# Optimization experiments

Hardware: AMD Instinct MI355X
Metric: run time of the kernel (lower is better)

The kernel has to match this reference:

```python
import jax, jax.numpy as jnp
import numpy as np

N_NODE = 50000
N_EDGE = 800000
D_FEAT = 64
DEPTH = 3
STEP = 0.5
AB_TUPLES = [(0.0, float(b)) for b in np.arange(0, 3, STEP)] + [(float(a), 0.0) for a in np.arange(STEP, 3, STEP)]
M = len(AB_TUPLES)  # 11 bases
L_INT, R_INT = -1.0, 1.0  # Jacobi spectral interval [l, r]


def setup_inputs() -> dict:
    key = jax.random.key(0)
    k1, k2, k3 = jax.random.split(key, 3)
    x = jax.random.normal(k1, (N_NODE, D_FEAT), dtype=jnp.float32)
    edge_index = jax.random.randint(k2, (2, N_EDGE), 0, N_NODE, dtype=jnp.int32)
    edge_attr = jax.random.uniform(k3, (N_EDGE,), dtype=jnp.float32)
    alphas = jnp.ones((DEPTH, M), dtype=jnp.float32)  # base_alpha = min(1/alpha, 1) = 1.0
    w = jnp.ones((1, M, 1, 1), dtype=jnp.float32)
    a_arr = jnp.array([t[0] for t in AB_TUPLES], dtype=jnp.float32)
    b_arr = jnp.array([t[1] for t in AB_TUPLES], dtype=jnp.float32)
    return {"x": x, "edge_index": edge_index, "edge_attr": edge_attr,
            "alphas": alphas, "w": w, "a_arr": a_arr, "b_arr": b_arr}


def _forward(x, edge_index, edge_attr, alphas, w, a_arr, b_arr):
    row, col = edge_index[0], edge_index[1]
    # gcn normalization: out-degree of row index, isolated nodes bumped to 1
    deg = jax.ops.segment_sum(jnp.ones_like(edge_attr), row, num_segments=N_NODE)
    deg = jnp.where(deg < 0.5, deg + 1.0, deg)
    dinv = deg ** -0.5
    val = dinv[row] * edge_attr * dinv[col]

    def spmm_all(xs):  # xs: [M, N, D] -> adj @ xs[m] for each basis (sequential map bounds memory)
        return jax.lax.map(
            lambda xm: jax.ops.segment_sum(val[:, None] * xm[col], row, num_segments=N_NODE), xs)

    a = a_arr[:, None, None]  # [M,1,1]
    b = b_arr[:, None, None]
    l, r = L_INT, R_INT
    xs0 = jnp.broadcast_to(x, (M,) + x.shape)  # order-0 term, shared across bases
    xs_hist = [xs0]
    # L = 1 Jacobi term
    coef1 = (a - b) / 2 - (a + b + 2) / 2 * (l + r) / (r - l)
    coef2 = (a + b + 2) / (r - l)
    al0 = alphas[0][:, None, None]
    xs_hist.append(al0 * (coef1 * xs0 + coef2 * spmm_all(xs0)))
    # L >= 2 three-term Jacobi recurrence
    for Lk in range(2, DEPTH + 1):
        Lf = float(Lk)
        coef_l = 2 * Lf * (Lf + a + b) * (2 * Lf - 2 + a + b)
        coef_lm1_1 = (2 * Lf + a + b - 1) * (2 * Lf + a + b) * (2 * Lf + a + b - 2)
        coef_lm1_2 = (2 * Lf + a + b - 1) * (a * a - b * b)
        coef_lm2 = 2 * (Lf - 1 + a) * (Lf - 1 + b) * (2 * Lf + a + b)
        alL = alphas[Lk - 1][:, None, None]
        alLm1 = alphas[Lk - 2][:, None, None]
        tmp1 = alL * (coef_lm1_1 / coef_l)
        tmp2 = alL * (coef_lm1_2 / coef_l)
        tmp3 = alL * alLm1 * (coef_lm2 / coef_l)
        tmp1_2 = tmp1 * (2 / (r - l))
        tmp2_2 = tmp1 * ((r + l) / (r - l)) + tmp2
        nx = tmp1_2 * spmm_all(xs_hist[-1]) - tmp2_2 * xs_hist[-1] - tmp3 * xs_hist[-2]
        xs_hist.append(nx)
    h = jnp.stack(xs_hist, axis=0)       # [K, M, N, D]
    h = jnp.transpose(h, (2, 1, 0, 3))   # [N, M, K, D], matches torch stack(dim=1) then stack(dim=2)
    return (w * h).sum(axis=1)           # [N, K, D]


def reference(x, edge_index, edge_attr, alphas, w, a_arr, b_arr):
    return _forward(x, edge_index, edge_attr, alphas, w, a_arr, b_arr)
```

## Files before the change

kernel.cpp:

```cpp
#include <hip/hip_runtime.h>
#include <hip/hip_fp16.h>

#define NN 50000
#define NE 800000
#define DF 64
#define MM 11
#define OUT_K 4
#define PAD 16
#define SLAB_CAP (NE + (PAD - 1) * NN + 64)

__device__ __forceinline__ float bf2f(unsigned short u) {
    union { unsigned int i; float f; } v; v.i = ((unsigned int)u) << 16; return v.f;
}
__device__ __forceinline__ unsigned short f2bf(float f) {
    union { float f; unsigned int i; } v; v.f = f;
    unsigned int u = v.i + 0x7FFFu + ((v.i >> 16) & 1u);
    return (unsigned short)(u >> 16);
}


__global__ void k_deg(const int* __restrict__ row, int* __restrict__ deg) {
    int e = blockIdx.x * blockDim.x + threadIdx.x;
    if (e < NE) atomicAdd(&deg[row[e]], 1);
}

__global__ void k_alloc(const int* __restrict__ deg, int* __restrict__ counter,
                        int* __restrict__ rowstart, float* __restrict__ dinv,
                        const float* __restrict__ alphas, const float* __restrict__ w,
                        const float* __restrict__ a_arr, const float* __restrict__ b_arr,
                        float* __restrict__ gamma) {
    int i = blockIdx.x * blockDim.x + threadIdx.x;
    int lane = threadIdx.x & 63;
    int d = (i < NN) ? deg[i] : 0;
    int dp = (d + PAD - 1) & ~(PAD - 1);
    int v = dp;
    #pragma unroll
    for (int off = 1; off < 64; off <<= 1) {
        int t = __shfl_up(v, off, 64);
        if (lane >= off) v += t;
    }
    int total = __shfl(v, 63, 64);
    int base = 0;
    if (lane == 63) base = atomicAdd(counter, total);
    base = __shfl(base, 63, 64);
    if (i < NN) {
        rowstart[i] = base + v - dp;
        dinv[i] = 1.0f / sqrtf((float)(d == 0 ? 1 : d));
    }
    if (i == 0) {
        float g[OUT_K][OUT_K];
        for (int k = 0; k < OUT_K; ++k)
            for (int j = 0; j < OUT_K; ++j) g[k][j] = 0.f;
        for (int m = 0; m < MM; ++m) {
            float a = a_arr[m], b = b_arr[m], wm = w[m];
            float c[OUT_K][OUT_K];
            for (int k = 0; k < OUT_K; ++k)
                for (int j = 0; j < OUT_K; ++j) c[k][j] = 0.f;
            c[0][0] = 1.f;
            float al0 = alphas[m];
            c[1][0] = al0 * 0.5f * (a - b);
            c[1][1] = al0 * 0.5f * (a + b + 2.f);
            for (int L = 2; L <= 3; ++L) {
                float Lf = (float)L;
                float alL = alphas[(L - 1) * MM + m];
                float alm = alphas[(L - 2) * MM + m];
                float ab = a + b;
                float t2L = 2.f * Lf + ab;
                float coef_l = 2.f * Lf * (Lf + ab) * (t2L - 2.f);
                float inv = 1.f / coef_l;
                float t1 = alL * ((t2L - 1.f) * t2L * (t2L - 2.f)) * inv;
                float t2 = alL * ((t2L - 1.f) * (a * a - b * b)) * inv;
                float t3 = alL * alm * (2.f * (Lf - 1.f + a) * (Lf - 1.f + b) * t2L) * inv;
                for (int j = 0; j < OUT_K; ++j) {
                    float ps = (j > 0) ? c[L - 1][j - 1] : 0.f;
                    c[L][j] = t1 * ps - t2 * c[L - 1][j] - t3 * c[L - 2][j];
                }
            }
            for (int k = 0; k < OUT_K; ++k)
                for (int j = 0; j < OUT_K; ++j) g[k][j] += wm * c[k][j];
        }
        for (int k = 0; k < OUT_K; ++k)
            for (int j = 0; j < OUT_K; ++j) gamma[k * OUT_K + j] = g[k][j];
    }
}

__global__ void k_fill_cast(const int* __restrict__ row, const int* __restrict__ col,
                            const float* __restrict__ ea, const float* __restrict__ dinv,
                            const int* __restrict__ rowstart, int* __restrict__ fill,
                            unsigned int* __restrict__ ecv,
                            const float* __restrict__ x, unsigned short* __restrict__ xb) {
    int t = blockIdx.x * blockDim.x + threadIdx.x;
    if (t < NE) {
        int r = row[t], c = col[t];
        int pos = rowstart[r] + atomicAdd(&fill[r], 1);
        float v = dinv[r] * ea[t] * dinv[c];
        unsigned short hb = __half_as_ushort(__float2half(v));
        ecv[pos] = (unsigned int)(unsigned short)c | ((unsigned int)hb << 16);
    } else {
        int j = t - NE;
        if (j < NN * DF) xb[j] = f2bf(x[j]);
    }
}

__device__ __forceinline__ float spmm_row(const unsigned int* __restrict__ ecv,
                                          int s, int n,
                                          const unsigned short* __restrict__ xin,
                                          int lane) {
    float acc = 0.f;
    for (int i = s; i < s + n; i += PAD) {
        unsigned int rec[PAD];
        #pragma unroll
        for (int j = 0; j < PAD; ++j) rec[j] = __builtin_nontemporal_load(&ecv[i + j]);
        unsigned short g[PAD];
        float vv[PAD];
        #pragma unroll
        for (int j = 0; j < PAD; ++j) {
            int c = (int)(rec[j] & 0xFFFFu);
            vv[j] = __half2float(__ushort_as_half((unsigned short)(rec[j] >> 16)));
            g[j] = xin[c * DF + lane];
        }
        #pragma unroll
        for (int j = 0; j < PAD; ++j) acc += vv[j] * bf2f(g[j]);
    }
    return acc;
}

__global__ __launch_bounds__(256) void k_spmm(
    const int* __restrict__ rowstart, const int* __restrict__ deg,
    const unsigned int* __restrict__ ecv, const unsigned short* __restrict__ xin,
    float* __restrict__ yout, unsigned short* __restrict__ bout) {
    int r = (blockIdx.x * blockDim.x + threadIdx.x) >> 6;
    int lane = threadIdx.x & 63;
    if (r >= NN) return;
    int s = rowstart[r];
    int n = (deg[r] + PAD - 1) & ~(PAD - 1);
    float acc = spmm_row(ecv, s, n, xin, lane);
    yout[r * DF + lane] = acc;
    bout[r * DF + lane] = f2bf(acc);
}

__global__ __launch_bounds__(256) void k_spmm_comb(
    const int* __restrict__ rowstart, const int* __restrict__ deg,
    const unsigned int* __restrict__ ecv, const unsigned short* __restrict__ xin,
    const float* __restrict__ x, const float* __restrict__ y1,
    const float* __restrict__ y2, const float* __restrict__ gamma,
    float* __restrict__ out) {
    int r = (blockIdx.x * blockDim.x + threadIdx.x) >> 6;
    int lane = threadIdx.x & 63;
    if (r >= NN) return;
    int s = rowstart[r];
    int n = (deg[r] + PAD - 1) & ~(PAD - 1);
    float v3 = spmm_row(ecv, s, n, xin, lane);
    int i = r * DF + lane;
    float v0 = x[i], v1 = y1[i], v2 = y2[i];
    float gm[OUT_K * OUT_K];
    #pragma unroll
    for (int t = 0; t < OUT_K * OUT_K; ++t) gm[t] = gamma[t];
    #pragma unroll
    for (int k = 0; k < OUT_K; ++k) {
        float o = gm[k * OUT_K + 0] * v0 + gm[k * OUT_K + 1] * v1 +
                  gm[k * OUT_K + 2] * v2 + gm[k * OUT_K + 3] * v3;
        out[(r * OUT_K + k) * DF + lane] = o;
    }
}


extern "C" void kernel_launch(void* const* d_in, const int* in_sizes, int n_in,
                              void* d_out, int out_size, void* d_ws, size_t ws_size,
                              hipStream_t stream) {
    const float* x      = (const float*)d_in[0];
    const int*   ei     = (const int*)d_in[1];
    const float* ea     = (const float*)d_in[2];
    const float* alphas = (const float*)d_in[3];
    const float* w      = (const float*)d_in[4];
    const float* a_arr  = (const float*)d_in[5];
    const float* b_arr  = (const float*)d_in[6];
    float* out = (float*)d_out;
    const int* row = ei;
    const int* col = ei + NE;

    char* ws = (char*)d_ws;
    size_t off = 0;
    auto alloc = [&](size_t bytes) {
        void* p = ws + off;
        off = (off + bytes + 255) & ~(size_t)255;
        return p;
    };
    int* deg      = (int*)alloc((size_t)(2 * NN + 1) * sizeof(int));
    int* fill     = deg + NN;
    int* counter  = deg + 2 * NN;
    unsigned int* ecv = (unsigned int*)alloc((size_t)SLAB_CAP * sizeof(unsigned int));
    size_t zero_end = off;
    int* rowstart = (int*)alloc((size_t)NN * sizeof(int));
    float* dinv   = (float*)alloc((size_t)NN * sizeof(float));
    unsigned short* xb0 = (unsigned short*)alloc((size_t)NN * DF * sizeof(unsigned short));
    unsigned short* xb1 = (unsigned short*)alloc((size_t)NN * DF * sizeof(unsigned short));
    unsigned short* xb2 = (unsigned short*)alloc((size_t)NN * DF * sizeof(unsigned short));
    float* y1 = (float*)alloc((size_t)NN * DF * sizeof(float));
    float* y2 = (float*)alloc((size_t)NN * DF * sizeof(float));
    float* gamma = (float*)alloc((size_t)OUT_K * OUT_K * sizeof(float));

    (void)hipMemsetAsync(deg, 0, zero_end, stream);

    k_deg<<<(NE + 255) / 256, 256, 0, stream>>>(row, deg);
    k_alloc<<<(NN + 255) / 256, 256, 0, stream>>>(deg, counter, rowstart, dinv,
                                                  alphas, w, a_arr, b_arr, gamma);
    k_fill_cast<<<(NE + NN * DF + 255) / 256, 256, 0, stream>>>(
        row, col, ea, dinv, rowstart, fill, ecv, x, xb0);

    int blocks = (NN + 3) / 4;
    k_spmm<<<blocks, 256, 0, stream>>>(rowstart, deg, ecv, xb0, y1, xb1);
    k_spmm<<<blocks, 256, 0, stream>>>(rowstart, deg, ecv, xb1, y2, xb2);
    k_spmm_comb<<<blocks, 256, 0, stream>>>(rowstart, deg, ecv, xb2, x, y1, y2,
                                            gamma, out);
}
```

Baseline: 273.7 us.

## Fuse all stages into one cooperative persistent kernel with grid syncs

Replaces the six separate kernel launches (degree count, row allocation, fill/cast, three SpMM passes) with a single cooperative kernel. Stages are separated by grid-wide barriers, and each stage uses grid-stride loops over a fixed grid sized from the occupancy query, capped at 1024 blocks. This removes per-launch overhead and inter-kernel gaps. In exchange, parallelism is limited to the resident grid, and each grid.sync adds barrier cost.

```diff
diff --git a/kernel.cpp b/kernel.cpp
--- a/kernel.cpp
+++ b/kernel.cpp
@@ -1,5 +1,8 @@
 #include <hip/hip_runtime.h>
 #include <hip/hip_fp16.h>
+#include <hip/hip_cooperative_groups.h>
+
+namespace cg = cooperative_groups;
 
 #define NN 50000
 #define NE 800000
@@ -18,48 +21,86 @@
     return (unsigned short)(u >> 16);
 }
 
-
-__global__ void k_deg(const int* __restrict__ row, int* __restrict__ deg) {
-    int e = blockIdx.x * blockDim.x + threadIdx.x;
-    if (e < NE) atomicAdd(&deg[row[e]], 1);
-}
-
-__global__ void k_alloc(const int* __restrict__ deg, int* __restrict__ counter,
-                        int* __restrict__ rowstart, float* __restrict__ dinv,
-                        const float* __restrict__ alphas, const float* __restrict__ w,
-                        const float* __restrict__ a_arr, const float* __restrict__ b_arr,
-                        float* __restrict__ gamma) {
-    int i = blockIdx.x * blockDim.x + threadIdx.x;
-    int lane = threadIdx.x & 63;
-    int d = (i < NN) ? deg[i] : 0;
-    int dp = (d + PAD - 1) & ~(PAD - 1);
-    int v = dp;
-    #pragma unroll
-    for (int off = 1; off < 64; off <<= 1) {
-        int t = __shfl_up(v, off, 64);
-        if (lane >= off) v += t;
-    }
-    int total = __shfl(v, 63, 64);
-    int base = 0;
-    if (lane == 63) base = atomicAdd(counter, total);
-    base = __shfl(base, 63, 64);
-    if (i < NN) {
-        rowstart[i] = base + v - dp;
-        dinv[i] = 1.0f / sqrtf((float)(d == 0 ? 1 : d));
-    }
-    if (i == 0) {
+__device__ __forceinline__ float spmm_row(const unsigned int* __restrict__ ecv,
+                                          int s, int n,
+                                          const unsigned short* __restrict__ xin,
+                                          int lane) {
+    float acc = 0.f;
+    for (int i = s; i < s + n; i += PAD) {
+        unsigned int rec[PAD];
+        #pragma unroll
+        for (int j = 0; j < PAD; ++j) rec[j] = __builtin_nontemporal_load(&ecv[i + j]);
+        unsigned short g[PAD];
+        float vv[PAD];
+        #pragma unroll
+        for (int j = 0; j < PAD; ++j) {
+            int c = (int)(rec[j] & 0xFFFFu);
+            vv[j] = __half2float(__ushort_as_half((unsigned short)(rec[j] >> 16)));
+            g[j] = xin[c * DF + lane];
+        }
+        #pragma unroll
+        for (int j = 0; j < PAD; ++j) acc += vv[j] * bf2f(g[j]);
+    }
+    return acc;
+}
+
+__global__ __launch_bounds__(256, 4) void k_mega(
+    const int* __restrict__ row, const int* __restrict__ col,
+    const float* __restrict__ ea, const float* __restrict__ alphas,
+    const float* __restrict__ w, const float* __restrict__ a_arr,
+    const float* __restrict__ b_arr, const float* __restrict__ x,
+    int* __restrict__ deg, int* __restrict__ counter, int* __restrict__ fill,
+    int* __restrict__ rowstart, float* __restrict__ dinv,
+    unsigned int* __restrict__ ecv,
+    unsigned short* __restrict__ xb0, unsigned short* __restrict__ xb1,
+    unsigned short* __restrict__ xb2,
+    float* __restrict__ y1, float* __restrict__ y2, float* __restrict__ gamma,
+    float* __restrict__ out) {
+    cg::grid_group grid = cg::this_grid();
+    const int tid = blockIdx.x * blockDim.x + threadIdx.x;
+    const int nth = gridDim.x * blockDim.x;
+    const int lane = threadIdx.x & 63;
+    const int wid = tid >> 6;
+    const int nw = nth >> 6;
+
+    for (int e = tid; e < NE; e += nth) atomicAdd(&deg[row[e]], 1);
+    grid.sync();
+
+    for (int i0 = wid * 64; i0 < NN; i0 += nw * 64) {
+        int i = i0 + lane;
+        int d = (i < NN) ? deg[i] : 0;
+        int dp = (d + PAD - 1) & ~(PAD - 1);
+        int v = dp;
+        #pragma unroll
+        for (int off = 1; off < 64; off <<= 1) {
+            int t = __shfl_up(v, off, 64);
+            if (lane >= off) v += t;
+        }
+        int total = __shfl(v, 63, 64);
+        int base = 0;
+        if (lane == 63) base = atomicAdd(counter, total);
+        base = __shfl(base, 63, 64);
+        if (i < NN) {
+            rowstart[i] = base + v - dp;
+            dinv[i] = 1.0f / sqrtf((float)(d == 0 ? 1 : d));
+        }
+    }
+    if (tid == 0) {
         float g[OUT_K][OUT_K];
+        #pragma unroll
         for (int k = 0; k < OUT_K; ++k)
+            #pragma unroll
             for (int j = 0; j < OUT_K; ++j) g[k][j] = 0.f;
         for (int m = 0; m < MM; ++m) {
             float a = a_arr[m], b = b_arr[m], wm = w[m];
-            float c[OUT_K][OUT_K];
-            for (int k = 0; k < OUT_K; ++k)
-                for (int j = 0; j < OUT_K; ++j) c[k][j] = 0.f;
-            c[0][0] = 1.f;
+            float c0[OUT_K], c1v[OUT_K], c2v[OUT_K], c3v[OUT_K];
+            #pragma unroll
+            for (int j = 0; j < OUT_K; ++j) { c0[j] = 0.f; c1v[j] = 0.f; c2v[j] = 0.f; c3v[j] = 0.f; }
+            c0[0] = 1.f;
             float al0 = alphas[m];
-            c[1][0] = al0 * 0.5f * (a - b);
-            c[1][1] = al0 * 0.5f * (a + b + 2.f);
+            c1v[0] = al0 * 0.5f * (a - b);
+            c1v[1] = al0 * 0.5f * (a + b + 2.f);
+            #pragma unroll
             for (int L = 2; L <= 3; ++L) {
                 float Lf = (float)L;
                 float alL = alphas[(L - 1) * MM + m];
@@ -71,96 +112,73 @@
                 float t1 = alL * ((t2L - 1.f) * t2L * (t2L - 2.f)) * inv;
                 float t2 = alL * ((t2L - 1.f) * (a * a - b * b)) * inv;
                 float t3 = alL * alm * (2.f * (Lf - 1.f + a) * (Lf - 1.f + b) * t2L) * inv;
-                for (int j = 0; j < OUT_K; ++j) {
-                    float ps = (j > 0) ? c[L - 1][j - 1] : 0.f;
-                    c[L][j] = t1 * ps - t2 * c[L - 1][j] - t3 * c[L - 2][j];
+                #pragma unroll
+                for (int j = OUT_K - 1; j >= 0; --j) {
+                    float ps, pc, pp;
+                    if (L == 2) { ps = (j > 0) ? c1v[j - 1] : 0.f; pc = c1v[j]; pp = c0[j]; }
+                    else        { ps = (j > 0) ? c2v[j - 1] : 0.f; pc = c2v[j]; pp = c1v[j]; }
+                    float nv = t1 * ps - t2 * pc - t3 * pp;
+                    if (L == 2) c2v[j] = nv; else c3v[j] = nv;
                 }
             }
-            for (int k = 0; k < OUT_K; ++k)
-                for (int j = 0; j < OUT_K; ++j) g[k][j] += wm * c[k][j];
-        }
+            #pragma unroll
+            for (int j = 0; j < OUT_K; ++j) {
+                g[0][j] += wm * c0[j];
+                g[1][j] += wm * c1v[j];
+                g[2][j] += wm * c2v[j];
+                g[3][j] += wm * c3v[j];
+            }
+        }
+        #pragma unroll
         for (int k = 0; k < OUT_K; ++k)
+            #pragma unroll
             for (int j = 0; j < OUT_K; ++j) gamma[k * OUT_K + j] = g[k][j];
     }
-}
-
-__global__ void k_fill_cast(const int* __restrict__ row, const int* __restrict__ col,
-                            const float* __restrict__ ea, const float* __restrict__ dinv,
-                            const int* __restrict__ rowstart, int* __restrict__ fill,
-                            unsigned int* __restrict__ ecv,
-                            const float* __restrict__ x, unsigned short* __restrict__ xb) {
-    int t = blockIdx.x * blockDim.x + threadIdx.x;
-    if (t < NE) {
-        int r = row[t], c = col[t];
+    grid.sync();
+
+    for (int e = tid; e < NE; e += nth) {
+        int r = row[e], c = col[e];
         int pos = rowstart[r] + atomicAdd(&fill[r], 1);
-        float v = dinv[r] * ea[t] * dinv[c];
+        float v = dinv[r] * ea[e] * dinv[c];
         unsigned short hb = __half_as_ushort(__float2half(v));
         ecv[pos] = (unsigned int)(unsigned short)c | ((unsigned int)hb << 16);
-    } else {
-        int j = t - NE;
-        if (j < NN * DF) xb[j] = f2bf(x[j]);
-    }
-}
-
-__device__ __forceinline__ float spmm_row(const unsigned int* __restrict__ ecv,
-                                          int s, int n,
-                                          const unsigned short* __restrict__ xin,
-                                          int lane) {
-    float acc = 0.f;
-    for (int i = s; i < s + n; i += PAD) {
-        unsigned int rec[PAD];
-        #pragma unroll
-        for (int j = 0; j < PAD; ++j) rec[j] = __builtin_nontemporal_load(&ecv[i + j]);
-        unsigned short g[PAD];
-        float vv[PAD];
-        #pragma unroll
-        for (int j = 0; j < PAD; ++j) {
-            int c = (int)(rec[j] & 0xFFFFu);
-            vv[j] = __half2float(__ushort_as_half((unsigned short)(rec[j] >> 16)));
-            g[j] = xin[c * DF + lane];
-        }
-        #pragma unroll
-        for (int j = 0; j < PAD; ++j) acc += vv[j] * bf2f(g[j]);
-    }
-    return acc;
-}
-
-__global__ __launch_bounds__(256) void k_spmm(
-    const int* __restrict__ rowstart, const int* __restrict__ deg,
-    const unsigned int* __restrict__ ecv, const unsigned short* __restrict__ xin,
-    float* __restrict__ yout, unsigned short* __restrict__ bout) {
-    int r = (blockIdx.x * blockDim.x + threadIdx.x) >> 6;
-    int lane = threadIdx.x & 63;
-    if (r >= NN) return;
-    int s = rowstart[r];
-    int n = (deg[r] + PAD - 1) & ~(PAD - 1);
-    float acc = spmm_row(ecv, s, n, xin, lane);
-    yout[r * DF + lane] = acc;
-    bout[r * DF + lane] = f2bf(acc);
-}
-
-__global__ __launch_bounds__(256) void k_spmm_comb(
-    const int* __restrict__ rowstart, const int* __restrict__ deg,
-    const unsigned int* __restrict__ ecv, const unsigned short* __restrict__ xin,
-    const float* __restrict__ x, const float* __restrict__ y1,
-    const float* __restrict__ y2, const float* __restrict__ gamma,
-    float* __restrict__ out) {
-    int r = (blockIdx.x * blockDim.x + threadIdx.x) >> 6;
-    int lane = threadIdx.x & 63;
-    if (r >= NN) return;
-    int s = rowstart[r];
-    int n = (deg[r] + PAD - 1) & ~(PAD - 1);
-    float v3 = spmm_row(ecv, s, n, xin, lane);
-    int i = r * DF + lane;
-    float v0 = x[i], v1 = y1[i], v2 = y2[i];
+    }
+    for (int i = tid; i < NN * DF; i += nth) xb0[i] = f2bf(x[i]);
+    grid.sync();
+
+    for (int r = wid; r < NN; r += nw) {
+        int s = rowstart[r];
+        int n = (deg[r] + PAD - 1) & ~(PAD - 1);
+        float acc = spmm_row(ecv, s, n, xb0, lane);
+        y1[r * DF + lane] = acc;
+        xb1[r * DF + lane] = f2bf(acc);
+    }
+    grid.sync();
+
+    for (int r = wid; r < NN; r += nw) {
+        int s = rowstart[r];
+        int n = (deg[r] + PAD - 1) & ~(PAD - 1);
+        float acc = spmm_row(ecv, s, n, xb1, lane);
+        y2[r * DF + lane] = acc;
+        xb2[r * DF + lane] = f2bf(acc);
+    }
+    grid.sync();
+
     float gm[OUT_K * OUT_K];
     #pragma unroll
     for (int t = 0; t < OUT_K * OUT_K; ++t) gm[t] = gamma[t];
-    #pragma unroll
-    for (int k = 0; k < OUT_K; ++k) {
-        float o = gm[k * OUT_K + 0] * v0 + gm[k * OUT_K + 1] * v1 +
-                  gm[k * OUT_K + 2] * v2 + gm[k * OUT_K + 3] * v3;
-        out[(r * OUT_K + k) * DF + lane] = o;
+    for (int r = wid; r < NN; r += nw) {
+        int s = rowstart[r];
+        int n = (deg[r] + PAD - 1) & ~(PAD - 1);
+        float v3 = spmm_row(ecv, s, n, xb2, lane);
+        int i = r * DF + lane;
+        float v0 = x[i], v1 = y1[i], v2 = y2[i];
+        #pragma unroll
+        for (int k = 0; k < OUT_K; ++k) {
+            float o = gm[k * OUT_K + 0] * v0 + gm[k * OUT_K + 1] * v1 +
+                      gm[k * OUT_K + 2] * v2 + gm[k * OUT_K + 3] * v3;
+            out[(r * OUT_K + k) * DF + lane] = o;
+        }
     }
 }
 
@@ -202,15 +220,19 @@
 
     (void)hipMemsetAsync(deg, 0, zero_end, stream);
 
-    k_deg<<<(NE + 255) / 256, 256, 0, stream>>>(row, deg);
-    k_alloc<<<(NN + 255) / 256, 256, 0, stream>>>(deg, counter, rowstart, dinv,
-                                                  alphas, w, a_arr, b_arr, gamma);
-    k_fill_cast<<<(NE + NN * DF + 255) / 256, 256, 0, stream>>>(
-        row, col, ea, dinv, rowstart, fill, ecv, x, xb0);
-
-    int blocks = (NN + 3) / 4;
-    k_spmm<<<blocks, 256, 0, stream>>>(rowstart, deg, ecv, xb0, y1, xb1);
-    k_spmm<<<blocks, 256, 0, stream>>>(rowstart, deg, ecv, xb1, y2, xb2);
-    k_spmm_comb<<<blocks, 256, 0, stream>>>(rowstart, deg, ecv, xb2, x, y1, y2,
-                                            gamma, out);
-}
+    int maxBlocksPerCU = 0;
+    (void)hipOccupancyMaxActiveBlocksPerMultiprocessor(&maxBlocksPerCU, k_mega, 256, 0);
+    if (maxBlocksPerCU < 1) maxBlocksPerCU = 1;
+    int gridBlocks = maxBlocksPerCU * 256;
+    if (gridBlocks > 1024) gridBlocks = 1024;
+
+    void* args[] = {
+        (void*)&row, (void*)&col, (void*)&ea, (void*)&alphas, (void*)&w,
+        (void*)&a_arr, (void*)&b_arr, (void*)&x,
+        (void*)&deg, (void*)&counter, (void*)&fill, (void*)&rowstart, (void*)&dinv,
+        (void*)&ecv, (void*)&xb0, (void*)&xb1, (void*)&xb2,
+        (void*)&y1, (void*)&y2, (void*)&gamma, (void*)&out
+    };
+    (void)hipLaunchCooperativeKernel((void*)k_mega, dim3(gridBlocks), dim3(256),
+                                     args, 0, stream);
+}
```

Result: slower. 632.2 us (+131.0%).
